# Optimization experiments

Hardware: AMD Instinct MI355X
Metric: run time of the kernel (lower is better)

The kernel has to match this reference:

```python
import jax, jax.numpy as jnp
import numpy as np
from functools import partial

# Thresholds from _SamAutomaticMaskGenerator defaults
MASK_THRESHOLD = 0.0
PRED_IOU_THRESH = 0.88
STABILITY_THRESH = 0.95
STABILITY_OFFSET = 1.0
BOX_NMS_THRESH = 0.7

N_MASKS, H, W = 1024, 256, 256  # 32x32 point grid -> 1024 masks; SAM low-res mask size


def setup_inputs() -> dict:
    key = jax.random.key(0)
    k1, k2, k3, k4, k5 = jax.random.split(key, 5)
    # Structured blob logits so stability scores / boxes / NMS behave realistically.
    cy = jax.random.uniform(k1, (N_MASKS,)) * H
    cx = jax.random.uniform(k2, (N_MASKS,)) * W
    r = 20.0 + jax.random.uniform(k3, (N_MASKS,)) * 60.0
    yy = jnp.arange(H, dtype=jnp.float32)[:, None]
    xx = jnp.arange(W, dtype=jnp.float32)[None, :]
    dist = jnp.sqrt((yy - cy[:, None, None]) ** 2 + (xx - cx[:, None, None]) ** 2)  # [N,H,W]
    noise = jax.random.normal(k4, (N_MASKS, H, W), dtype=jnp.float32) * 0.1
    mask_logits = (2.0 * (r[:, None, None] - dist) + noise).astype(jnp.float32)
    iou_preds = jax.random.uniform(k5, (N_MASKS,), dtype=jnp.float32)
    return {"mask_logits": mask_logits, "iou_preds": iou_preds}


def _masks_to_boxes(binary):
    # binary: [N,H,W] bool -> inclusive xyxy boxes [N,4] float32 (empty masks -> zeros),
    # matching SAM's batched_mask_to_box.
    n, h, w = binary.shape
    row_any = binary.any(axis=2)  # [N,H]
    col_any = binary.any(axis=1)  # [N,W]
    ys = jnp.arange(h)
    xs = jnp.arange(w)
    top = jnp.min(jnp.where(row_any, ys, h), axis=1)
    bottom = jnp.max(jnp.where(row_any, ys, -1), axis=1)
    left = jnp.min(jnp.where(col_any, xs, w), axis=1)
    right = jnp.max(jnp.where(col_any, xs, -1), axis=1)
    boxes = jnp.stack([left, top, right, bottom], axis=-1).astype(jnp.float32)
    empty = ~row_any.any(axis=1)
    return jnp.where(empty[:, None], 0.0, boxes)


def _box_iou_one_vs_all(box, boxes):
    # box: [4], boxes: [N,4] xyxy -> iou [N]
    x0 = jnp.maximum(box[0], boxes[:, 0])
    y0 = jnp.maximum(box[1], boxes[:, 1])
    x1 = jnp.minimum(box[2], boxes[:, 2])
    y1 = jnp.minimum(box[3], boxes[:, 3])
    inter = jnp.clip(x1 - x0, 0.0) * jnp.clip(y1 - y0, 0.0)
    area_a = jnp.clip(box[2] - box[0], 0.0) * jnp.clip(box[3] - box[1], 0.0)
    area_b = jnp.clip(boxes[:, 2] - boxes[:, 0], 0.0) * jnp.clip(boxes[:, 3] - boxes[:, 1], 0.0)
    return inter / jnp.maximum(area_a + area_b - inter, 1e-6)


def _greedy_nms(boxes, scores, valid, thresh):
    # Greedy NMS over fixed N, returning a keep mask in original order.
    n = boxes.shape[0]
    order = jnp.argsort(-jnp.where(valid, scores, -jnp.inf))
    b = boxes[order]
    keep0 = valid[order]
    idx = jnp.arange(n)

    def body(i, keep):
        iou = _box_iou_one_vs_all(b[i], b)
        suppress = (iou > thresh) & (idx > i) & keep[i]
        return keep & ~suppress

    keep_sorted = jax.lax.fori_loop(0, n, body, keep0)
    return jnp.zeros((n,), dtype=bool).at[order].set(keep_sorted)


def reference(mask_logits, iou_preds):
    # Stability score: area at (thr+offset) / area at (thr-offset), as in SAM.
    hi = (mask_logits > (MASK_THRESHOLD + STABILITY_OFFSET)).sum(axis=(1, 2)).astype(jnp.float32)
    lo = (mask_logits > (MASK_THRESHOLD - STABILITY_OFFSET)).sum(axis=(1, 2)).astype(jnp.float32)
    stability = hi / jnp.maximum(lo, 1.0)

    binary = mask_logits > MASK_THRESHOLD  # [N,H,W] bool
    valid = (iou_preds > PRED_IOU_THRESH) & (stability >= STABILITY_THRESH)

    boxes = _masks_to_boxes(binary)  # [N,4]
    keep = _greedy_nms(boxes, iou_preds, valid, BOX_NMS_THRESH)  # [N] bool

    # Differentiable summary output: soft masks gated by kept score.
    gated = iou_preds * keep.astype(mask_logits.dtype)  # [N]
    out = jax.nn.sigmoid(mask_logits) * gated[:, None, None]  # [N,H,W]
    return out, keep, boxes
```

## Files before the change

kernel.cpp:

```cpp
#include <hip/hip_runtime.h>
#include <math.h>

#define NMASK 1024
#define HH 256
#define WW 256
#define HW 65536
#define OUT_ELEMS 67108864

__global__ __launch_bounds__(256) void stats_kernel(
    const float* __restrict__ logits, int* __restrict__ stats) {
  const int m = blockIdx.x;
  const int t = threadIdx.x;
  const float4* __restrict__ p = (const float4*)(logits + (size_t)m * HW);

  int hi = 0, lo = 0;
  int miny = HH, maxy = -1, minx = WW, maxx = -1;

  for (int k = 0; k < 64; ++k) {
    const int f = k * 256 + t;
    const float4 v = p[f];
    const int y = f >> 6;
    const int x0 = (f & 63) << 2;

    const bool p0 = v.x > 0.0f, p1 = v.y > 0.0f, p2 = v.z > 0.0f, p3 = v.w > 0.0f;
    hi += (v.x > 1.0f) + (v.y > 1.0f) + (v.z > 1.0f) + (v.w > 1.0f);
    lo += (v.x > -1.0f) + (v.y > -1.0f) + (v.z > -1.0f) + (v.w > -1.0f);
    if (p0 | p1 | p2 | p3) {
      miny = min(miny, y);
      maxy = max(maxy, y);
      if (p0) { minx = min(minx, x0);     maxx = max(maxx, x0); }
      if (p1) { minx = min(minx, x0 + 1); maxx = max(maxx, x0 + 1); }
      if (p2) { minx = min(minx, x0 + 2); maxx = max(maxx, x0 + 2); }
      if (p3) { minx = min(minx, x0 + 3); maxx = max(maxx, x0 + 3); }
    }
  }

  for (int off = 32; off; off >>= 1) {
    hi += __shfl_down(hi, off);
    lo += __shfl_down(lo, off);
    miny = min(miny, __shfl_down(miny, off));
    maxy = max(maxy, __shfl_down(maxy, off));
    minx = min(minx, __shfl_down(minx, off));
    maxx = max(maxx, __shfl_down(maxx, off));
  }

  __shared__ int red[4][6];
  const int wv = t >> 6, ln = t & 63;
  if (ln == 0) {
    red[wv][0] = hi;  red[wv][1] = lo;
    red[wv][2] = miny; red[wv][3] = maxy;
    red[wv][4] = minx; red[wv][5] = maxx;
  }
  __syncthreads();
  if (t == 0) {
    int H2 = 0, L2 = 0, mny = HH, mxy = -1, mnx = WW, mxx = -1;
    for (int w = 0; w < 4; ++w) {
      H2 += red[w][0]; L2 += red[w][1];
      mny = min(mny, red[w][2]); mxy = max(mxy, red[w][3]);
      mnx = min(mnx, red[w][4]); mxx = max(mxx, red[w][5]);
    }
    int* s = stats + m * 8;
    s[0] = H2; s[1] = L2; s[2] = mny; s[3] = mxy; s[4] = mnx; s[5] = mxx;
  }
}

__global__ __launch_bounds__(1024) void score_kernel(
    const float* __restrict__ iou_preds, const int* __restrict__ stats,
    float* __restrict__ score, int* __restrict__ validA,
    float* __restrict__ boxf, int* __restrict__ nvalid,
    float* __restrict__ boxes_out) {
  __shared__ int cnt;
  const int i = threadIdx.x;
  if (i == 0) cnt = 0;
  __syncthreads();

  const int* s = stats + i * 8;
  const int hi = s[0], lo = s[1], mny = s[2], mxy = s[3], mnx = s[4], mxx = s[5];
  const float stab = (float)hi / fmaxf((float)lo, 1.0f);
  const float iv = iou_preds[i];
  const bool valid = (iv > 0.88f) && (stab >= 0.95f);

  float bx0, by0, bx1, by1;
  if (mxy < 0) { bx0 = by0 = bx1 = by1 = 0.0f; }
  else { bx0 = (float)mnx; by0 = (float)mny; bx1 = (float)mxx; by1 = (float)mxy; }

  boxf[i * 4 + 0] = bx0; boxf[i * 4 + 1] = by0;
  boxf[i * 4 + 2] = bx1; boxf[i * 4 + 3] = by1;
  boxes_out[i * 4 + 0] = bx0; boxes_out[i * 4 + 1] = by0;
  boxes_out[i * 4 + 2] = bx1; boxes_out[i * 4 + 3] = by1;

  score[i] = valid ? iv : -INFINITY;
  validA[i] = valid ? 1 : 0;
  if (valid) atomicAdd(&cnt, 1);
  __syncthreads();
  if (i == 0) *nvalid = cnt;
}

__global__ __launch_bounds__(256) void rank_kernel(
    const float* __restrict__ score, const int* __restrict__ validA,
    const float* __restrict__ boxf, float* __restrict__ sbox,
    int* __restrict__ sidx, int* __restrict__ svalid) {
  const int i = blockIdx.x;
  const int t = threadIdx.x;
  const float si = score[i];
  int r = 0;
  for (int j = t; j < NMASK; j += 256) {
    const float sj = score[j];
    r += (sj > si) || (sj == si && j < i);
  }
  for (int off = 32; off; off >>= 1) r += __shfl_down(r, off);
  __shared__ int red[4];
  if ((t & 63) == 0) red[t >> 6] = r;
  __syncthreads();
  if (t == 0) {
    const int rank = red[0] + red[1] + red[2] + red[3];
    sidx[rank] = i;
    svalid[rank] = validA[i];
    sbox[rank * 4 + 0] = boxf[i * 4 + 0];
    sbox[rank * 4 + 1] = boxf[i * 4 + 1];
    sbox[rank * 4 + 2] = boxf[i * 4 + 2];
    sbox[rank * 4 + 3] = boxf[i * 4 + 3];
  }
}

__global__ __launch_bounds__(1024) void iou_kernel(
    const float* __restrict__ sbox, const int* __restrict__ nvalid,
    unsigned long long* __restrict__ rows) {
  const int i = blockIdx.x;
  if (i >= *nvalid) return;
  const int j = threadIdx.x;
  const float ax0 = sbox[i * 4 + 0], ay0 = sbox[i * 4 + 1];
  const float ax1 = sbox[i * 4 + 2], ay1 = sbox[i * 4 + 3];
  const float bx0 = sbox[j * 4 + 0], by0 = sbox[j * 4 + 1];
  const float bx1 = sbox[j * 4 + 2], by1 = sbox[j * 4 + 3];
  const float x0 = fmaxf(ax0, bx0), y0 = fmaxf(ay0, by0);
  const float x1 = fminf(ax1, bx1), y1 = fminf(ay1, by1);
  const float inter = fmaxf(x1 - x0, 0.0f) * fmaxf(y1 - y0, 0.0f);
  const float aa = fmaxf(ax1 - ax0, 0.0f) * fmaxf(ay1 - ay0, 0.0f);
  const float ab = fmaxf(bx1 - bx0, 0.0f) * fmaxf(by1 - by0, 0.0f);
  const float iou = inter / fmaxf(aa + ab - inter, 1e-6f);
  const bool supp = (iou > 0.7f) && (j > i);
  const unsigned long long b = __ballot(supp);
  if ((j & 63) == 0) rows[i * 16 + (j >> 6)] = b;
}

#define PREF_ROWS 256
__global__ __launch_bounds__(256) void nms_kernel(
    const int* __restrict__ nvalid, const unsigned long long* __restrict__ rows,
    const int* __restrict__ sidx, const int* __restrict__ svalid,
    const float* __restrict__ iou_preds, float* __restrict__ gated,
    float* __restrict__ keep_out) {
  __shared__ unsigned long long srows[PREF_ROWS * 16];
  const int nv = *nvalid;
  const int t = threadIdx.x;
  const int pref = min(nv, PREF_ROWS) * 16;
  for (int k = t; k < pref; k += 256) srows[k] = rows[k];
  __syncthreads();
  if (t >= 64) return;
  const int lane = t;

  unsigned long long keepword = 0ull;
  for (int c = 0; c < 16; ++c) {
    const int v = svalid[c * 64 + lane];
    const unsigned long long b = __ballot(v != 0);
    if (lane == c) keepword = b;
  }

  for (int i = 0; i < nv; ++i) {
    const int w = i >> 6, bit = i & 63;
    const unsigned long long kw = __shfl(keepword, w, 64);
    if ((kw >> bit) & 1ull) {
      if (lane < 16) {
        const unsigned long long r =
            (i < PREF_ROWS) ? srows[i * 16 + lane] : rows[i * 16 + lane];
        keepword &= ~r;
      }
    }
  }

  for (int c = 0; c < 16; ++c) {
    const unsigned long long kw = __shfl(keepword, c, 64);
    const int j = c * 64 + lane;
    const int orig = sidx[j];
    const float kept = ((kw >> lane) & 1ull) ? 1.0f : 0.0f;
    keep_out[orig] = kept;
    gated[orig] = kept * iou_preds[orig];
  }
}

__global__ __launch_bounds__(256) void out_kernel(
    const float* __restrict__ logits, const float* __restrict__ gated,
    float* __restrict__ out) {
  const int b = blockIdx.x;
  const int m = b >> 4;
  const float g = gated[m];
  const size_t base4 = (size_t)m * 16384 + (size_t)(b & 15) * 1024;
  const float4* __restrict__ in4 = (const float4*)logits + base4;
  float4* __restrict__ o4 = (float4*)out + base4;
  const int t = threadIdx.x;
  if (g == 0.0f) {
    const float4 z = {0.0f, 0.0f, 0.0f, 0.0f};
    o4[t] = z; o4[t + 256] = z; o4[t + 512] = z; o4[t + 768] = z;
  } else {
#pragma unroll
    for (int k = 0; k < 4; ++k) {
      const float4 v = in4[t + k * 256];
      float4 r;
      r.x = g / (1.0f + __expf(-v.x));
      r.y = g / (1.0f + __expf(-v.y));
      r.z = g / (1.0f + __expf(-v.z));
      r.w = g / (1.0f + __expf(-v.w));
      o4[t + k * 256] = r;
    }
  }
}

extern "C" void kernel_launch(void* const* d_in, const int* in_sizes, int n_in,
                              void* d_out, int out_size, void* d_ws, size_t ws_size,
                              hipStream_t stream) {
  const float* logits = (const float*)d_in[0];
  const float* iou    = (const float*)d_in[1];

  float* out       = (float*)d_out;
  float* keep_out  = out + OUT_ELEMS;
  float* boxes_out = keep_out + NMASK;

  char* w = (char*)d_ws;
  int*   stats  = (int*)(w);
  float* score  = (float*)(w + 32768);
  int*   validA = (int*)(w + 36864);
  float* boxf   = (float*)(w + 40960);
  int*   nvalid = (int*)(w + 57344);
  float* sbox   = (float*)(w + 57408);
  int*   sidx   = (int*)(w + 73792);
  int*   svalid = (int*)(w + 77888);
  float* gated  = (float*)(w + 81984);
  unsigned long long* rows = (unsigned long long*)(w + 86080);

  stats_kernel<<<NMASK, 256, 0, stream>>>(logits, stats);
  score_kernel<<<1, 1024, 0, stream>>>(iou, stats, score, validA, boxf, nvalid, boxes_out);
  rank_kernel<<<NMASK, 256, 0, stream>>>(score, validA, boxf, sbox, sidx, svalid);
  iou_kernel<<<NMASK, 1024, 0, stream>>>(sbox, nvalid, rows);
  nms_kernel<<<1, 256, 0, stream>>>(nvalid, rows, sidx, svalid, iou, gated, keep_out);
  out_kernel<<<NMASK * 16, 256, 0, stream>>>(logits, gated, out);
}
```

Baseline: 468.5 us.

## Fuse score, rank, IoU and NMS into stats plus one block kernel

Folds the per-mask score and box computation into the stats kernel's final reduction. Replaces the separate rank, IoU-matrix and NMS kernels with a single 1024-thread block that compacts valid masks, ranks only those, builds the suppression bitmask in shared memory, and runs the greedy scan. The goal is to cut launch count and global round trips between the small serial stages. The cost is that all of the NMS work now runs on one workgroup, and rows beyond 256 are recomputed inside the scan.

```diff
diff --git a/kernel.cpp b/kernel.cpp
--- a/kernel.cpp
+++ b/kernel.cpp
@@ -8,7 +8,9 @@
 #define OUT_ELEMS 67108864
 
 __global__ __launch_bounds__(256) void stats_kernel(
-    const float* __restrict__ logits, int* __restrict__ stats) {
+    const float* __restrict__ logits, const float* __restrict__ iou_preds,
+    float* __restrict__ score, float* __restrict__ boxf,
+    float* __restrict__ boxes_out) {
   const int m = blockIdx.x;
   const int t = threadIdx.x;
   const float4* __restrict__ p = (const float4*)(logits + (size_t)m * HW);
@@ -59,133 +61,143 @@
       mny = min(mny, red[w][2]); mxy = max(mxy, red[w][3]);
       mnx = min(mnx, red[w][4]); mxx = max(mxx, red[w][5]);
     }
-    int* s = stats + m * 8;
-    s[0] = H2; s[1] = L2; s[2] = mny; s[3] = mxy; s[4] = mnx; s[5] = mxx;
-  }
-}
-
-__global__ __launch_bounds__(1024) void score_kernel(
-    const float* __restrict__ iou_preds, const int* __restrict__ stats,
-    float* __restrict__ score, int* __restrict__ validA,
-    float* __restrict__ boxf, int* __restrict__ nvalid,
-    float* __restrict__ boxes_out) {
-  __shared__ int cnt;
-  const int i = threadIdx.x;
-  if (i == 0) cnt = 0;
-  __syncthreads();
-
-  const int* s = stats + i * 8;
-  const int hi = s[0], lo = s[1], mny = s[2], mxy = s[3], mnx = s[4], mxx = s[5];
-  const float stab = (float)hi / fmaxf((float)lo, 1.0f);
-  const float iv = iou_preds[i];
-  const bool valid = (iv > 0.88f) && (stab >= 0.95f);
-
-  float bx0, by0, bx1, by1;
-  if (mxy < 0) { bx0 = by0 = bx1 = by1 = 0.0f; }
-  else { bx0 = (float)mnx; by0 = (float)mny; bx1 = (float)mxx; by1 = (float)mxy; }
-
-  boxf[i * 4 + 0] = bx0; boxf[i * 4 + 1] = by0;
-  boxf[i * 4 + 2] = bx1; boxf[i * 4 + 3] = by1;
-  boxes_out[i * 4 + 0] = bx0; boxes_out[i * 4 + 1] = by0;
-  boxes_out[i * 4 + 2] = bx1; boxes_out[i * 4 + 3] = by1;
-
-  score[i] = valid ? iv : -INFINITY;
-  validA[i] = valid ? 1 : 0;
-  if (valid) atomicAdd(&cnt, 1);
-  __syncthreads();
-  if (i == 0) *nvalid = cnt;
-}
-
-__global__ __launch_bounds__(256) void rank_kernel(
-    const float* __restrict__ score, const int* __restrict__ validA,
-    const float* __restrict__ boxf, float* __restrict__ sbox,
-    int* __restrict__ sidx, int* __restrict__ svalid) {
-  const int i = blockIdx.x;
-  const int t = threadIdx.x;
-  const float si = score[i];
-  int r = 0;
-  for (int j = t; j < NMASK; j += 256) {
-    const float sj = score[j];
-    r += (sj > si) || (sj == si && j < i);
-  }
-  for (int off = 32; off; off >>= 1) r += __shfl_down(r, off);
-  __shared__ int red[4];
-  if ((t & 63) == 0) red[t >> 6] = r;
-  __syncthreads();
-  if (t == 0) {
-    const int rank = red[0] + red[1] + red[2] + red[3];
-    sidx[rank] = i;
-    svalid[rank] = validA[i];
-    sbox[rank * 4 + 0] = boxf[i * 4 + 0];
-    sbox[rank * 4 + 1] = boxf[i * 4 + 1];
-    sbox[rank * 4 + 2] = boxf[i * 4 + 2];
-    sbox[rank * 4 + 3] = boxf[i * 4 + 3];
-  }
-}
-
-__global__ __launch_bounds__(1024) void iou_kernel(
-    const float* __restrict__ sbox, const int* __restrict__ nvalid,
-    unsigned long long* __restrict__ rows) {
-  const int i = blockIdx.x;
-  if (i >= *nvalid) return;
-  const int j = threadIdx.x;
-  const float ax0 = sbox[i * 4 + 0], ay0 = sbox[i * 4 + 1];
-  const float ax1 = sbox[i * 4 + 2], ay1 = sbox[i * 4 + 3];
-  const float bx0 = sbox[j * 4 + 0], by0 = sbox[j * 4 + 1];
-  const float bx1 = sbox[j * 4 + 2], by1 = sbox[j * 4 + 3];
-  const float x0 = fmaxf(ax0, bx0), y0 = fmaxf(ay0, by0);
-  const float x1 = fminf(ax1, bx1), y1 = fminf(ay1, by1);
-  const float inter = fmaxf(x1 - x0, 0.0f) * fmaxf(y1 - y0, 0.0f);
-  const float aa = fmaxf(ax1 - ax0, 0.0f) * fmaxf(ay1 - ay0, 0.0f);
-  const float ab = fmaxf(bx1 - bx0, 0.0f) * fmaxf(by1 - by0, 0.0f);
-  const float iou = inter / fmaxf(aa + ab - inter, 1e-6f);
-  const bool supp = (iou > 0.7f) && (j > i);
-  const unsigned long long b = __ballot(supp);
-  if ((j & 63) == 0) rows[i * 16 + (j >> 6)] = b;
-}
-
-#define PREF_ROWS 256
-__global__ __launch_bounds__(256) void nms_kernel(
-    const int* __restrict__ nvalid, const unsigned long long* __restrict__ rows,
-    const int* __restrict__ sidx, const int* __restrict__ svalid,
+    const float stab = (float)H2 / fmaxf((float)L2, 1.0f);
+    const float iv = iou_preds[m];
+    const bool valid = (iv > 0.88f) && (stab >= 0.95f);
+
+    float4 b;
+    if (mxy < 0) { b.x = b.y = b.z = b.w = 0.0f; }
+    else { b.x = (float)mnx; b.y = (float)mny; b.z = (float)mxx; b.w = (float)mxy; }
+
+    ((float4*)boxf)[m] = b;
+    ((float4*)boxes_out)[m] = b;
+    score[m] = valid ? iv : -INFINITY;
+  }
+}
+
+__global__ __launch_bounds__(1024) void nms_fused(
+    const float* __restrict__ score_g, const float* __restrict__ boxf,
     const float* __restrict__ iou_preds, float* __restrict__ gated,
     float* __restrict__ keep_out) {
-  __shared__ unsigned long long srows[PREF_ROWS * 16];
-  const int nv = *nvalid;
+  __shared__ float s_score[NMASK];
+  __shared__ float4 s_bo[NMASK];
+  __shared__ int s_sidx[NMASK];
+  __shared__ int s_rank[NMASK];
+  __shared__ unsigned long long s_rows[256 * 16];
+  __shared__ int s_wcnt[16];
+  __shared__ int s_woff[16];
+  __shared__ int s_nv;
+  __shared__ unsigned long long s_keepw[16];
+
   const int t = threadIdx.x;
-  const int pref = min(nv, PREF_ROWS) * 16;
-  for (int k = t; k < pref; k += 256) srows[k] = rows[k];
-  __syncthreads();
-  if (t >= 64) return;
-  const int lane = t;
-
-  unsigned long long keepword = 0ull;
-  for (int c = 0; c < 16; ++c) {
-    const int v = svalid[c * 64 + lane];
-    const unsigned long long b = __ballot(v != 0);
-    if (lane == c) keepword = b;
-  }
-
-  for (int i = 0; i < nv; ++i) {
-    const int w = i >> 6, bit = i & 63;
-    const unsigned long long kw = __shfl(keepword, w, 64);
-    if ((kw >> bit) & 1ull) {
-      if (lane < 16) {
-        const unsigned long long r =
-            (i < PREF_ROWS) ? srows[i * 16 + lane] : rows[i * 16 + lane];
-        keepword &= ~r;
+  const int wv = t >> 6, lane = t & 63;
+
+  const float sc = score_g[t];
+  s_score[t] = sc;
+  s_bo[t] = ((const float4*)boxf)[t];
+  const bool valid = sc != -INFINITY;
+  const unsigned long long vb = __ballot(valid);
+  if (lane == 0) s_wcnt[wv] = __popcll(vb);
+  __syncthreads();
+  if (t == 0) {
+    int acc = 0;
+    for (int w = 0; w < 16; ++w) { s_woff[w] = acc; acc += s_wcnt[w]; }
+    s_nv = acc;
+  }
+  __syncthreads();
+  const int nv = s_nv;
+  int* cidx = (int*)s_rows;
+  const unsigned long long below = lane ? (~0ull >> (64 - lane)) : 0ull;
+  const int vbelow = s_woff[wv] + __popcll(vb & below);
+  if (valid) {
+    cidx[vbelow] = t;
+  } else {
+    const int r = nv + (t - vbelow);
+    s_rank[t] = r;
+    s_sidx[r] = t;
+  }
+  __syncthreads();
+
+  if (t < nv) {
+    const int i = cidx[t];
+    const float si = s_score[i];
+    int r = 0;
+    for (int q = 0; q < nv; ++q) {
+      const int j = cidx[q];
+      const float sj = s_score[j];
+      r += (sj > si) || (sj == si && j < i);
+    }
+    s_rank[i] = r;
+    s_sidx[r] = i;
+  }
+  __syncthreads();
+
+  const int R = min(nv, 256);
+  const int nw = (nv + 63) >> 6;
+  for (int k = t; k < R * 16; k += 1024) s_rows[k] = 0ull;
+  __syncthreads();
+  for (int i = wv; i < R; i += 16) {
+    const float4 a = s_bo[s_sidx[i]];
+    const float aa = fmaxf(a.z - a.x, 0.0f) * fmaxf(a.w - a.y, 0.0f);
+    for (int cw = 0; cw < nw; ++cw) {
+      const int col = cw * 64 + lane;
+      bool supp = false;
+      if (col < nv && col > i) {
+        const float4 b = s_bo[s_sidx[col]];
+        const float x0 = fmaxf(a.x, b.x), y0 = fmaxf(a.y, b.y);
+        const float x1 = fminf(a.z, b.z), y1 = fminf(a.w, b.w);
+        const float inter = fmaxf(x1 - x0, 0.0f) * fmaxf(y1 - y0, 0.0f);
+        const float ab = fmaxf(b.z - b.x, 0.0f) * fmaxf(b.w - b.y, 0.0f);
+        const float iou = inter / fmaxf(aa + ab - inter, 1e-6f);
+        supp = iou > 0.7f;
       }
-    }
-  }
-
-  for (int c = 0; c < 16; ++c) {
-    const unsigned long long kw = __shfl(keepword, c, 64);
-    const int j = c * 64 + lane;
-    const int orig = sidx[j];
-    const float kept = ((kw >> lane) & 1ull) ? 1.0f : 0.0f;
-    keep_out[orig] = kept;
-    gated[orig] = kept * iou_preds[orig];
-  }
+      const unsigned long long bal = __ballot(supp);
+      if (lane == 0) s_rows[i * 16 + cw] = bal;
+    }
+  }
+  __syncthreads();
+
+  if (wv == 0) {
+    unsigned long long keepword;
+    {
+      const int base = lane * 64;
+      keepword = (nv >= base + 64) ? ~0ull
+               : (nv <= base ? 0ull : ((1ull << (nv - base)) - 1ull));
+    }
+    for (int i = 0; i < nv; ++i) {
+      const unsigned long long kw = __shfl(keepword, i >> 6, 64);
+      if (!((kw >> (i & 63)) & 1ull)) continue;
+      if (i < 256) {
+        if (lane < 16) keepword &= ~s_rows[i * 16 + lane];
+      } else {
+        const float4 a = s_bo[s_sidx[i]];
+        const float aa = fmaxf(a.z - a.x, 0.0f) * fmaxf(a.w - a.y, 0.0f);
+        unsigned long long clr = 0ull;
+        for (int cw = 0; cw < nw; ++cw) {
+          const int col = cw * 64 + lane;
+          bool supp = false;
+          if (col < nv && col > i) {
+            const float4 b = s_bo[s_sidx[col]];
+            const float x0 = fmaxf(a.x, b.x), y0 = fmaxf(a.y, b.y);
+            const float x1 = fminf(a.z, b.z), y1 = fminf(a.w, b.w);
+            const float inter = fmaxf(x1 - x0, 0.0f) * fmaxf(y1 - y0, 0.0f);
+            const float ab = fmaxf(b.z - b.x, 0.0f) * fmaxf(b.w - b.y, 0.0f);
+            supp = inter / fmaxf(aa + ab - inter, 1e-6f) > 0.7f;
+          }
+          const unsigned long long bal = __ballot(supp);
+          if (lane == cw) clr = bal;
+        }
+        keepword &= ~clr;
+      }
+    }
+    if (lane < 16) s_keepw[lane] = keepword;
+  }
+  __syncthreads();
+
+  const int r = s_rank[t];
+  const float kept = ((s_keepw[r >> 6] >> (r & 63)) & 1ull) ? 1.0f : 0.0f;
+  keep_out[t] = kept;
+  gated[t] = kept * iou_preds[t];
 }
 
 __global__ __launch_bounds__(256) void out_kernel(
@@ -226,21 +238,11 @@
   float* boxes_out = keep_out + NMASK;
 
   char* w = (char*)d_ws;
-  int*   stats  = (int*)(w);
-  float* score  = (float*)(w + 32768);
-  int*   validA = (int*)(w + 36864);
-  float* boxf   = (float*)(w + 40960);
-  int*   nvalid = (int*)(w + 57344);
-  float* sbox   = (float*)(w + 57408);
-  int*   sidx   = (int*)(w + 73792);
-  int*   svalid = (int*)(w + 77888);
-  float* gated  = (float*)(w + 81984);
-  unsigned long long* rows = (unsigned long long*)(w + 86080);
-
-  stats_kernel<<<NMASK, 256, 0, stream>>>(logits, stats);
-  score_kernel<<<1, 1024, 0, stream>>>(iou, stats, score, validA, boxf, nvalid, boxes_out);
-  rank_kernel<<<NMASK, 256, 0, stream>>>(score, validA, boxf, sbox, sidx, svalid);
-  iou_kernel<<<NMASK, 1024, 0, stream>>>(sbox, nvalid, rows);
-  nms_kernel<<<1, 256, 0, stream>>>(nvalid, rows, sidx, svalid, iou, gated, keep_out);
+  float* score = (float*)(w);
+  float* boxf  = (float*)(w + 4096);
+  float* gated = (float*)(w + 20480);
+
+  stats_kernel<<<NMASK, 256, 0, stream>>>(logits, iou, score, boxf, boxes_out);
+  nms_fused<<<1, 1024, 0, stream>>>(score, boxf, iou, gated, keep_out);
   out_kernel<<<NMASK * 16, 256, 0, stream>>>(logits, gated, out);
 }
```

New measurement: 463.7 us. About the same (-1.0%).
